# Kernel optimization log

Measured on AMD Instinct MI355X. Metric: run time of the kernel, lower is better.

## Reference

```python
import jax, jax.numpy as jnp
import numpy as np

B_SZ, NX, IN_DIM = 32, 16384, 3
DIM, J, MODE, RANK, FC_DIM, OUT_DIM, N_LAYERS = 64, 16, 128, 4, 128, 1, 3


def setup_inputs() -> dict:
    key = jax.random.key(0)
    ks = jax.random.split(key, 20)
    scale = 1.0 / (MODE * MODE)
    s_out = 1.0 / MODE
    x = jax.random.normal(ks[0], (B_SZ, NX, IN_DIM), jnp.float32)
    bases = jax.random.normal(ks[1], (NX, MODE), jnp.float32) / np.sqrt(NX)
    wbases = jax.random.normal(ks[2], (NX, MODE), jnp.float32) / np.sqrt(NX)
    product = bases.T @ wbases  # (MODE_out, MODE_in)
    D_out = np.sqrt(s_out) * jax.random.uniform(ks[3], (J, MODE), jnp.float32)
    D_in = np.sqrt(s_out) * jax.random.uniform(ks[4], (J, MODE), jnp.float32)
    A = s_out * jax.random.uniform(ks[5], (J, RANK, MODE), jnp.float32)
    Bm = s_out * jax.random.uniform(ks[6], (J, RANK, MODE), jnp.float32)
    W_sp = scale * jax.random.normal(ks[7], (N_LAYERS, DIM, DIM, J), jnp.float32)
    W_conv = jax.random.normal(ks[8], (N_LAYERS, DIM, DIM), jnp.float32) / np.sqrt(DIM)
    b_conv = jnp.zeros((N_LAYERS, DIM), jnp.float32)
    W0 = jax.random.normal(ks[9], (IN_DIM, DIM), jnp.float32) / np.sqrt(IN_DIM)
    b0 = jnp.zeros((DIM,), jnp.float32)
    W1 = jax.random.normal(ks[10], (DIM, FC_DIM), jnp.float32) / np.sqrt(DIM)
    b1 = jnp.zeros((FC_DIM,), jnp.float32)
    W2 = jax.random.normal(ks[11], (FC_DIM, OUT_DIM), jnp.float32) / np.sqrt(FC_DIM)
    b2 = jnp.zeros((OUT_DIM,), jnp.float32)
    return {"x": x, "bases": bases, "wbases": wbases, "product": product,
            "D_out": D_out, "D_in": D_in, "A": A, "Bm": Bm,
            "W_sp": W_sp, "W_conv": W_conv, "b_conv": b_conv,
            "W0": W0, "b0": b0, "W1": W1, "b1": b1, "W2": W2, "b2": b2}


def reference(x, bases, wbases, product, D_out, D_in, A, Bm, W_sp, W_conv, b_conv,
              W0, b0, W1, b1, W2, b2):
    # fc0: (b, nx, in_dim) -> (b, nx, dim), then channel-first (b, dim, nx)
    h = jnp.swapaxes(x @ W0 + b0, 1, 2)
    # H construction: diag outer-products + low-rank A^T B update (mask_mode=0 so full add)
    H = D_out[:, :, None] * D_in[:, None, :] * product[None] \
        + jnp.einsum('jrk,jrl->jkl', A, Bm)  # (J, MODE, MODE)
    for i in range(N_LAYERS):
        xh = jnp.einsum('bcx,xk->bck', h, wbases)          # spectral transform
        xh1 = jnp.einsum('jkl,bil->bijk', H, xh)           # H mixing
        y = jnp.einsum('ioj,bijk->bok', W_sp[i], xh1)      # channel/kernel contraction
        x1 = jnp.einsum('bck,xk->bcx', y, bases)           # inverse transform
        x2 = jnp.einsum('oc,bcx->box', W_conv[i], h) + b_conv[i][None, :, None]
        h = x1 + x2
        if i != N_LAYERS - 1:
            h = jax.nn.gelu(h, approximate=False)
    h = jnp.swapaxes(h, 1, 2)  # (b, nx, dim)
    h = jax.nn.gelu(h @ W1 + b1, approximate=False)
    return h @ W2 + b2
```

## Files before the change

kernel.cpp:

```cpp
#include <hip/hip_runtime.h>
#include <hip/hip_bf16.h>
#include <math.h>

#define B_SZ   32
#define NXX    16384
#define IN_DIM 3
#define DIM    64
#define JM     16
#define MODE   128
#define RANKK  4
#define FC_DIM 128
#define N_LAY  3

typedef __attribute__((ext_vector_type(8))) short bf16x8;
typedef __attribute__((ext_vector_type(4))) float f32x4;
typedef unsigned short u16;

__device__ __forceinline__ float gelu_fast(float v) {
    float p = v * (0.7978845608f + 0.0356774081f * v * v);
    float e = __expf(-2.f * p);
    return v * __builtin_amdgcn_rcpf(1.f + e);
}
__device__ __forceinline__ u16 to_bf16(float v) {
    __hip_bfloat16 b = __float2bfloat16(v);
    return *(u16*)&b;
}

__global__ __launch_bounds__(256) void k_zero(float* __restrict__ p, int n) {
    int i = blockIdx.x * 256 + threadIdx.x;
    if (i < n) p[i] = 0.f;
}

__global__ __launch_bounds__(256) void k_build_H(
        const float* __restrict__ Dout, const float* __restrict__ Din,
        const float* __restrict__ product, const float* __restrict__ A,
        const float* __restrict__ Bm, u16* __restrict__ Hbf) {
    int idx = blockIdx.x * 256 + threadIdx.x;
    int j = idx >> 14;
    int k = (idx >> 7) & 127;
    int l = idx & 127;
    float v = Dout[j * MODE + k] * Din[j * MODE + l] * product[k * MODE + l];
#pragma unroll
    for (int r = 0; r < RANKK; ++r)
        v += A[(j * RANKK + r) * MODE + k] * Bm[(j * RANKK + r) * MODE + l];
    Hbf[idx] = to_bf16(v);
}

__global__ __launch_bounds__(256) void k_setup_wst(
        const float* __restrict__ Wsp, u16* __restrict__ WsT) {
    int idx = blockIdx.x * 256 + threadIdx.x;
    int i = idx & 63, o = (idx >> 6) & 63, j = (idx >> 12) & 15, lay = idx >> 16;
    WsT[idx] = to_bf16(Wsp[(((size_t)lay * 64 + i) * 64 + o) * 16 + j]);
}

__global__ __launch_bounds__(256) void k_setup_bases(
        const float* __restrict__ bases, u16* __restrict__ bh) {
    int idx = blockIdx.x * 256 + threadIdx.x;
    int x = idx >> 7, k = idx & 127;
    size_t off = (size_t)(k >> 3) * 131072 + (size_t)x * 8 + (k & 7);
    bh[off] = to_bf16(bases[idx]);
}

__global__ __launch_bounds__(256) void k_setup_wbT(
        const float* __restrict__ wb, u16* __restrict__ Th) {
    __shared__ float tile[32][33];
    int bx = blockIdx.x, bl = blockIdx.y;
    int t = threadIdx.x;
    int i = t >> 5, jj = t & 31;
#pragma unroll
    for (int r = 0; r < 4; ++r)
        tile[i + r * 8][jj] = wb[(size_t)(bx * 32 + i + r * 8) * MODE + bl * 32 + jj];
    __syncthreads();
#pragma unroll
    for (int r = 0; r < 4; ++r) {
        int l = bl * 32 + i + r * 8;
        int x = bx * 32 + jj;
        Th[(size_t)l * NXX + x] = to_bf16(tile[jj][i + r * 8]);
    }
}

__global__ __launch_bounds__(256) void k_setup_w1t(
        const float* __restrict__ W1, u16* __restrict__ wh) {
    int i = blockIdx.x * 256 + threadIdx.x;
    int f = i >> 6, c = i & 63;
    wh[i] = to_bf16(W1[c * FC_DIM + f]);
}

__global__ __launch_bounds__(256) void k_fc0(
        const float* __restrict__ x, const float* __restrict__ W0,
        const float* __restrict__ b0, u16* __restrict__ hh) {
    __shared__ float w0s[IN_DIM * DIM + DIM];
    int t = threadIdx.x;
    if (t < IN_DIM * DIM) w0s[t] = W0[t];
    if (t < DIM) w0s[IN_DIM * DIM + t] = b0[t];
    __syncthreads();
    int b = blockIdx.y;
    int xi = blockIdx.x * 32 + (t >> 3);
    int c8 = (t & 7) * 8;
    const float* xp = x + ((size_t)b * NXX + xi) * IN_DIM;
    float x0 = xp[0], x1 = xp[1], x2 = xp[2];
    u16 rh[8];
#pragma unroll
    for (int i = 0; i < 8; ++i) {
        int c = c8 + i;
        float v = x0 * w0s[c] + x1 * w0s[DIM + c] + x2 * w0s[2 * DIM + c]
                + w0s[3 * DIM + c];
        rh[i] = to_bf16(v);
    }
    size_t o = ((size_t)(b << 14) + xi) * 64 + c8;
    *(ushort4*)(hh + o)     = make_ushort4(rh[0], rh[1], rh[2], rh[3]);
    *(ushort4*)(hh + o + 4) = make_ushort4(rh[4], rh[5], rh[6], rh[7]);
}

#define SPAD 72
__global__ __launch_bounds__(256) void k_spectral_mfma(
        const u16* __restrict__ Hh,
        const u16* __restrict__ Wh,
        float* __restrict__ xh) {
    __shared__ u16 Ash[64 * SPAD];
    int t = threadIdx.x;
    int wave = t >> 6, lane = t & 63, quad = lane >> 4, l16 = lane & 15;
    int b = blockIdx.x;
    int x0 = blockIdx.y * 512;
    int cq = (t & 15) * 4;
    int xq = (t >> 4) * 4;
    int colw = (xq + ((t & 7) << 3)) & 63;
    const u16* srch = Hh + ((size_t)(b << 14) + x0 + xq) * 64 + cq;
    int l0 = wave * 32;
    const u16* w0h = Wh + (size_t)(l0 + l16) * NXX + x0;
    const u16* w1h = Wh + (size_t)(l0 + 16 + l16) * NXX + x0;
    f32x4 acc[4][2] = {};
    for (int kt = 0; kt < 512; kt += 64) {
        __syncthreads();
        {
            const u16* s = srch + (size_t)kt * 64;
            ushort4 r0 = *(const ushort4*)(s);
            ushort4 r1 = *(const ushort4*)(s + 64);
            ushort4 r2 = *(const ushort4*)(s + 128);
            ushort4 r3 = *(const ushort4*)(s + 192);
            *(ushort4*)&Ash[(cq + 0) * SPAD + colw] = make_ushort4(r0.x, r1.x, r2.x, r3.x);
            *(ushort4*)&Ash[(cq + 1) * SPAD + colw] = make_ushort4(r0.y, r1.y, r2.y, r3.y);
            *(ushort4*)&Ash[(cq + 2) * SPAD + colw] = make_ushort4(r0.z, r1.z, r2.z, r3.z);
            *(ushort4*)&Ash[(cq + 3) * SPAD + colw] = make_ushort4(r0.w, r1.w, r2.w, r3.w);
        }
        __syncthreads();
#pragma unroll
        for (int k0 = 0; k0 < 64; k0 += 32) {
            bf16x8 afh[4];
#pragma unroll
            for (int ct = 0; ct < 4; ++ct) {
                int rr = ct * 16 + l16;
                int ro = rr * SPAD + (((k0 + quad * 8) + (((rr >> 2) & 7) << 3)) & 63);
                afh[ct] = *(const bf16x8*)&Ash[ro];
            }
            int go = kt + k0 + quad * 8;
            bf16x8 b0h = *(const bf16x8*)(w0h + go);
            bf16x8 b1h = *(const bf16x8*)(w1h + go);
#pragma unroll
            for (int ct = 0; ct < 4; ++ct) {
                acc[ct][0] = __builtin_amdgcn_mfma_f32_16x16x32_bf16(afh[ct], b0h, acc[ct][0], 0, 0, 0);
                acc[ct][1] = __builtin_amdgcn_mfma_f32_16x16x32_bf16(afh[ct], b1h, acc[ct][1], 0, 0, 0);
            }
        }
    }
    float* xb = xh + (size_t)(b << 6) * 128;
#pragma unroll
    for (int ct = 0; ct < 4; ++ct)
#pragma unroll
        for (int lt = 0; lt < 2; ++lt)
#pragma unroll
            for (int r = 0; r < 4; ++r)
                atomicAdd(xb + (size_t)(ct * 16 + quad * 4 + r) * 128 + l0 + lt * 16 + l16,
                          acc[ct][lt][r]);
}

#define XPAD 136
#define TPAD 72
__global__ __launch_bounds__(256) void k_hmix_mfma(
        const float* __restrict__ xh, const u16* __restrict__ Hbf,
        const u16* __restrict__ WsT, float* __restrict__ y, int lay) {
    __shared__ u16 xsb[64 * XPAD];
    __shared__ u16 Ts[128 * TPAD];
    int t = threadIdx.x;
    int wave = t >> 6, lane = t & 63, quad = lane >> 4, l16 = lane & 15;
    int b = blockIdx.x, j = blockIdx.y;
    const float* xb = xh + (size_t)b * DIM * MODE;
    for (int idx = t; idx < DIM * MODE; idx += 256)
        xsb[(idx >> 7) * XPAD + (idx & 127)] = to_bf16(xb[idx]);
    __syncthreads();
    int k_base = wave * 32;
    {
        f32x4 acc[2][4] = {};
        const u16* Hj = Hbf + (size_t)j * MODE * MODE;
#pragma unroll
        for (int l0 = 0; l0 < 128; l0 += 32) {
            bf16x8 af[2], bf[4];
#pragma unroll
            for (int mt = 0; mt < 2; ++mt)
                af[mt] = *(const bf16x8*)(Hj + (size_t)(k_base + mt * 16 + l16) * 128 + l0 + quad * 8);
#pragma unroll
            for (int nt = 0; nt < 4; ++nt)
                bf[nt] = *(const bf16x8*)&xsb[(nt * 16 + l16) * XPAD + l0 + quad * 8];
#pragma unroll
            for (int mt = 0; mt < 2; ++mt)
#pragma unroll
                for (int nt = 0; nt < 4; ++nt)
                    acc[mt][nt] = __builtin_amdgcn_mfma_f32_16x16x32_bf16(af[mt], bf[nt], acc[mt][nt], 0, 0, 0);
        }
#pragma unroll
        for (int mt = 0; mt < 2; ++mt)
#pragma unroll
            for (int nt = 0; nt < 4; ++nt)
#pragma unroll
                for (int r = 0; r < 4; ++r)
                    Ts[(k_base + mt * 16 + quad * 4 + r) * TPAD + nt * 16 + l16] =
                        to_bf16(acc[mt][nt][r]);
    }
    __syncthreads();
    {
        f32x4 acc[4][2] = {};
        const u16* Wj = WsT + ((size_t)lay * JM + j) * DIM * DIM;
#pragma unroll
        for (int i0 = 0; i0 < 64; i0 += 32) {
            bf16x8 af[4], bf[2];
#pragma unroll
            for (int mt = 0; mt < 4; ++mt)
                af[mt] = *(const bf16x8*)(Wj + (size_t)(mt * 16 + l16) * 64 + i0 + quad * 8);
#pragma unroll
            for (int nt = 0; nt < 2; ++nt)
                bf[nt] = *(const bf16x8*)&Ts[(k_base + nt * 16 + l16) * TPAD + i0 + quad * 8];
#pragma unroll
            for (int mt = 0; mt < 4; ++mt)
#pragma unroll
                for (int nt = 0; nt < 2; ++nt)
                    acc[mt][nt] = __builtin_amdgcn_mfma_f32_16x16x32_bf16(af[mt], bf[nt], acc[mt][nt], 0, 0, 0);
        }
        float* yb = y + (size_t)b * DIM * MODE;
#pragma unroll
        for (int mt = 0; mt < 4; ++mt)
#pragma unroll
            for (int nt = 0; nt < 2; ++nt)
#pragma unroll
                for (int r = 0; r < 4; ++r)
                    atomicAdd(yb + (size_t)(mt * 16 + quad * 4 + r) * 128 + k_base + nt * 16 + l16,
                              acc[mt][nt][r]);
    }
}

__global__ __launch_bounds__(256) void k_build_A(
        const float* __restrict__ y, const float* __restrict__ Wconv,
        u16* __restrict__ Ah, int lay) {
    int b = blockIdx.x;
    for (int idx = threadIdx.x; idx < 12288; idx += 256) {
        int i = idx & 7, l16 = (idx >> 3) & 15, quad = (idx >> 7) & 3,
            ot = (idx >> 9) & 3, ks = idx >> 11;
        int o = ot * 16 + l16;
        int k = ks * 32 + quad * 8 + i;
        float v = (k < 128) ? y[((size_t)b * DIM + o) * MODE + k]
                            : Wconv[(size_t)lay * DIM * DIM + o * DIM + (k - 128)];
        Ah[(size_t)b * 12288 + idx] = to_bf16(v);
    }
}

template <bool DO_MLP>
__global__ __launch_bounds__(256, 4) void k_inv_conv_mfma(
        const u16* __restrict__ Afh,
        const u16* __restrict__ Bfh,
        u16* __restrict__ Hh,
        const float* __restrict__ bconv, int lay,
        const u16* __restrict__ W1h,
        const float* __restrict__ b1, const float* __restrict__ W2,
        const float* __restrict__ b2, float* __restrict__ out) {
    __shared__ u16 Ash[12288];
    __shared__ u16 hsh[128 * 64];
    int t = threadIdx.x;
    int wave = t >> 6, lane = t & 63, quad = lane >> 4, l16 = lane & 15;
    int bid = blockIdx.x;
    int swz = (bid & 7) * 512 + (bid >> 3);
    int b = swz & 31;
    int x0 = (swz >> 5) * 128;

    const u16* afb = Afh + (size_t)b * 12288;
#pragma unroll
    for (int i = 0; i < 6; ++i) {
        int idx = i * 256 + t;
        *(bf16x8*)&Ash[idx * 8] = *(const bf16x8*)(afb + (size_t)idx * 8);
    }
#pragma unroll
    for (int it = 0; it < 4; ++it) {
        int idx = it * 256 + t;
        int row = idx >> 3, c8 = (idx & 7) * 8;
        size_t src = ((size_t)(b << 14) + x0 + row) * 64 + c8;
        *(bf16x8*)&hsh[row * 64 + (c8 ^ ((row & 7) << 3))] =
            *(const bf16x8*)(Hh + src);
    }
    __syncthreads();

    int xw = wave * 32;
    bf16x8 bglob[4][2];
#pragma unroll
    for (int ks = 0; ks < 4; ++ks)
#pragma unroll
        for (int x2 = 0; x2 < 2; ++x2) {
            int xl = xw + x2 * 16 + l16;
            size_t bo = (size_t)((ks * 4 + quad) * 16384 + x0 + xl) * 8;
            bglob[ks][x2] = *(const bf16x8*)(Bfh + bo);
        }

    f32x4 acc[4][2] = {};
#pragma unroll
    for (int ks = 0; ks < 6; ++ks) {
        bf16x8 afh[4], bfh[2];
#pragma unroll
        for (int x2 = 0; x2 < 2; ++x2) {
            if (ks < 4) {
                bfh[x2] = bglob[ks][x2];
            } else {
                int xl = xw + x2 * 16 + l16;
                int ko = (ks - 4) * 32 + quad * 8;
                bfh[x2] = *(const bf16x8*)&hsh[xl * 64 + (ko ^ ((xl & 7) << 3))];
            }
        }
#pragma unroll
        for (int ot = 0; ot < 4; ++ot)
            afh[ot] = *(const bf16x8*)&Ash[(((ks * 4 + ot) * 4 + quad) * 16 + l16) * 8];
#pragma unroll
        for (int ot = 0; ot < 4; ++ot)
#pragma unroll
            for (int x2 = 0; x2 < 2; ++x2)
                acc[ot][x2] = __builtin_amdgcn_mfma_f32_16x16x32_bf16(
                    afh[ot], bfh[x2], acc[ot][x2], 0, 0, 0);
    }

#pragma unroll
    for (int ot = 0; ot < 4; ++ot) {
        float4 bc = *(const float4*)(bconv + lay * DIM + ot * 16 + quad * 4);
#pragma unroll
        for (int x2 = 0; x2 < 2; ++x2) {
            int xl = xw + x2 * 16 + l16;
            float vr[4] = {acc[ot][x2][0] + bc.x, acc[ot][x2][1] + bc.y,
                           acc[ot][x2][2] + bc.z, acc[ot][x2][3] + bc.w};
            if (!DO_MLP) {
#pragma unroll
                for (int r = 0; r < 4; ++r) vr[r] = gelu_fast(vr[r]);
            }
            ushort4 uh;
            uh.x = to_bf16(vr[0]); uh.y = to_bf16(vr[1]);
            uh.z = to_bf16(vr[2]); uh.w = to_bf16(vr[3]);
            int col = ot * 16 + quad * 4;
            *(ushort4*)&hsh[xl * 64 + (col ^ ((xl & 7) << 3))] = uh;
        }
    }

    if (!DO_MLP) {
        __syncthreads();
#pragma unroll
        for (int it = 0; it < 4; ++it) {
            int idx = it * 256 + t;
            int row = idx >> 3, c8 = (idx & 7) * 8;
            size_t dst = ((size_t)(b << 14) + x0 + row) * 64 + c8;
            *(bf16x8*)(Hh + dst) =
                *(const bf16x8*)&hsh[row * 64 + (c8 ^ ((row & 7) << 3))];
        }
        return;
    }

#pragma unroll
    for (int x2 = 0; x2 < 2; ++x2) {
        int xl = xw + x2 * 16 + l16;
        bf16x8 ah[2];
#pragma unroll
        for (int ks = 0; ks < 2; ++ks) {
            int ko = ks * 32 + quad * 8;
            ah[ks] = *(const bf16x8*)&hsh[xl * 64 + (ko ^ ((xl & 7) << 3))];
        }
        float vo[4] = {0.f, 0.f, 0.f, 0.f};
#pragma unroll
        for (int ft = 0; ft < 8; ++ft) {
            f32x4 a2 = {};
#pragma unroll
            for (int ks = 0; ks < 2; ++ks) {
                size_t o = (size_t)(ft * 16 + l16) * 64 + ks * 32 + quad * 8;
                bf16x8 bh = *(const bf16x8*)(W1h + o);
                a2 = __builtin_amdgcn_mfma_f32_16x16x32_bf16(ah[ks], bh, a2, 0, 0, 0);
            }
            float bb = b1[ft * 16 + l16];
            float w2 = W2[ft * 16 + l16];
#pragma unroll
            for (int r = 0; r < 4; ++r)
                vo[r] += gelu_fast(a2[r] + bb) * w2;
        }
#pragma unroll
        for (int r = 0; r < 4; ++r) {
            float v = vo[r];
            v += __shfl_xor(v, 1);
            v += __shfl_xor(v, 2);
            v += __shfl_xor(v, 4);
            v += __shfl_xor(v, 8);
            vo[r] = v;
        }
        if (l16 == 0) {
            float bb2 = b2[0];
            float4 o4 = make_float4(vo[0] + bb2, vo[1] + bb2,
                                    vo[2] + bb2, vo[3] + bb2);
            *(float4*)(out + (size_t)b * NXX + x0 + xw + x2 * 16 + quad * 4) = o4;
        }
    }
}

extern "C" void kernel_launch(void* const* d_in, const int* in_sizes, int n_in,
                              void* d_out, int out_size, void* d_ws, size_t ws_size,
                              hipStream_t stream) {
    const float* x      = (const float*)d_in[0];
    const float* bases  = (const float*)d_in[1];
    const float* wbases = (const float*)d_in[2];
    const float* product= (const float*)d_in[3];
    const float* Dout   = (const float*)d_in[4];
    const float* Din    = (const float*)d_in[5];
    const float* A      = (const float*)d_in[6];
    const float* Bm     = (const float*)d_in[7];
    const float* Wsp    = (const float*)d_in[8];
    const float* Wconv  = (const float*)d_in[9];
    const float* bconv  = (const float*)d_in[10];
    const float* W0     = (const float*)d_in[11];
    const float* b0     = (const float*)d_in[12];
    const float* W1     = (const float*)d_in[13];
    const float* b1     = (const float*)d_in[14];
    const float* W2     = (const float*)d_in[15];
    const float* b2     = (const float*)d_in[16];
    float* out = (float*)d_out;

    const size_t need = 79314944;
    if (ws_size < need) {
        k_zero<<<dim3((out_size + 255) / 256), dim3(256), 0, stream>>>(out, out_size);
        return;
    }

    char* W = (char*)d_ws;
    size_t off = 0;
    auto alloc = [&](size_t bytes) { void* p = W + off; off += bytes; return p; };
    u16*   Hbf      = (u16*)alloc(524288);
    u16*   WsT      = (u16*)alloc(393216);
    u16*   bases_hi = (u16*)alloc(4194304);
    u16*   wbT_hi   = (u16*)alloc(4194304);
    u16*   Abuf_hi  = (u16*)alloc(786432);
    float* ybuf     = (float*)alloc(1048576);
    float* xh       = (float*)alloc(1048576);
    u16*   h_hi     = (u16*)alloc(67108864);
    u16*   w1t_hi   = (u16*)alloc(16384);

    k_build_H<<<dim3(1024), dim3(256), 0, stream>>>(Dout, Din, product, A, Bm, Hbf);
    k_setup_wst<<<dim3(768), dim3(256), 0, stream>>>(Wsp, WsT);
    k_setup_bases<<<dim3(8192), dim3(256), 0, stream>>>(bases, bases_hi);
    k_setup_wbT<<<dim3(512, 4), dim3(256), 0, stream>>>(wbases, wbT_hi);
    k_setup_w1t<<<dim3(32), dim3(256), 0, stream>>>(W1, w1t_hi);
    k_fc0<<<dim3(512, B_SZ), dim3(256), 0, stream>>>(x, W0, b0, h_hi);

    for (int lay = 0; lay < N_LAY; ++lay) {
        int last = (lay == N_LAY - 1);
        k_zero<<<dim3(2048), dim3(256), 0, stream>>>(ybuf, 524288);
        k_spectral_mfma<<<dim3(B_SZ, 32), dim3(256), 0, stream>>>(
            h_hi, wbT_hi, xh);
        k_hmix_mfma<<<dim3(B_SZ, JM), dim3(256), 0, stream>>>(
            xh, Hbf, WsT, ybuf, lay);
        k_build_A<<<dim3(B_SZ), dim3(256), 0, stream>>>(ybuf, Wconv, Abuf_hi, lay);
        dim3 g(4096), blk(256);
        if (last)
            k_inv_conv_mfma<true><<<g, blk, 0, stream>>>(
                Abuf_hi, bases_hi, h_hi, bconv, lay,
                w1t_hi, b1, W2, b2, out);
        else
            k_inv_conv_mfma<false><<<g, blk, 0, stream>>>(
                Abuf_hi, bases_hi, h_hi, bconv, lay,
                w1t_hi, b1, W2, b2, out);
    }
}
```

Measured before the change: 473.9 us.

## Fuse H-mixing with A-buffer build and double-tile the inverse conv kernel

The H-mixing kernel now loops over all 16 kernel indices inside one block per batch. It accumulates y in registers and writes the bf16 A-operand layout directly, which removes the y atomics, the y zeroing kernel and the separate k_build_A launch. The inverse-transform/conv kernel now handles two 128-column tiles per block. It loads the h operand straight from global memory into registers and prefetches the second tile while the first tile's epilogue runs. The trade-off is that H-mixing drops to only 32 blocks running a serial j loop, which may leave most compute units idle, and xh is now zeroed explicitly before the spectral step.

```diff
diff --git a/kernel.cpp b/kernel.cpp
--- a/kernel.cpp
+++ b/kernel.cpp
@@ -176,90 +176,86 @@
 
 #define XPAD 136
 #define TPAD 72
-__global__ __launch_bounds__(256) void k_hmix_mfma(
+__global__ __launch_bounds__(256) void k_hmix2(
         const float* __restrict__ xh, const u16* __restrict__ Hbf,
-        const u16* __restrict__ WsT, float* __restrict__ y, int lay) {
+        const u16* __restrict__ WsT, const float* __restrict__ Wconv,
+        u16* __restrict__ Ah, int lay) {
     __shared__ u16 xsb[64 * XPAD];
     __shared__ u16 Ts[128 * TPAD];
     int t = threadIdx.x;
     int wave = t >> 6, lane = t & 63, quad = lane >> 4, l16 = lane & 15;
-    int b = blockIdx.x, j = blockIdx.y;
+    int b = blockIdx.x;
     const float* xb = xh + (size_t)b * DIM * MODE;
     for (int idx = t; idx < DIM * MODE; idx += 256)
         xsb[(idx >> 7) * XPAD + (idx & 127)] = to_bf16(xb[idx]);
+    for (int idx = 8192 + t; idx < 12288; idx += 256) {
+        int i = idx & 7, ll = (idx >> 3) & 15, qq = (idx >> 7) & 3,
+            ot = (idx >> 9) & 3, ks = idx >> 11;
+        int o = ot * 16 + ll;
+        int k = ks * 32 + qq * 8 + i;
+        Ah[(size_t)b * 12288 + idx] =
+            to_bf16(Wconv[(size_t)lay * DIM * DIM + o * DIM + (k - 128)]);
+    }
     __syncthreads();
     int k_base = wave * 32;
-    {
-        f32x4 acc[2][4] = {};
-        const u16* Hj = Hbf + (size_t)j * MODE * MODE;
-#pragma unroll
-        for (int l0 = 0; l0 < 128; l0 += 32) {
-            bf16x8 af[2], bf[4];
+    f32x4 accy[4][2] = {};
+    for (int j = 0; j < JM; ++j) {
+        {
+            f32x4 acc[2][4] = {};
+            const u16* Hj = Hbf + (size_t)j * MODE * MODE;
+#pragma unroll
+            for (int l0 = 0; l0 < 128; l0 += 32) {
+                bf16x8 af[2], bf[4];
+#pragma unroll
+                for (int mt = 0; mt < 2; ++mt)
+                    af[mt] = *(const bf16x8*)(Hj + (size_t)(k_base + mt * 16 + l16) * 128 + l0 + quad * 8);
+#pragma unroll
+                for (int nt = 0; nt < 4; ++nt)
+                    bf[nt] = *(const bf16x8*)&xsb[(nt * 16 + l16) * XPAD + l0 + quad * 8];
+#pragma unroll
+                for (int mt = 0; mt < 2; ++mt)
+#pragma unroll
+                    for (int nt = 0; nt < 4; ++nt)
+                        acc[mt][nt] = __builtin_amdgcn_mfma_f32_16x16x32_bf16(af[mt], bf[nt], acc[mt][nt], 0, 0, 0);
+            }
 #pragma unroll
             for (int mt = 0; mt < 2; ++mt)
-                af[mt] = *(const bf16x8*)(Hj + (size_t)(k_base + mt * 16 + l16) * 128 + l0 + quad * 8);
-#pragma unroll
-            for (int nt = 0; nt < 4; ++nt)
-                bf[nt] = *(const bf16x8*)&xsb[(nt * 16 + l16) * XPAD + l0 + quad * 8];
-#pragma unroll
-            for (int mt = 0; mt < 2; ++mt)
 #pragma unroll
                 for (int nt = 0; nt < 4; ++nt)
-                    acc[mt][nt] = __builtin_amdgcn_mfma_f32_16x16x32_bf16(af[mt], bf[nt], acc[mt][nt], 0, 0, 0);
-        }
-#pragma unroll
-        for (int mt = 0; mt < 2; ++mt)
-#pragma unroll
-            for (int nt = 0; nt < 4; ++nt)
-#pragma unroll
-                for (int r = 0; r < 4; ++r)
-                    Ts[(k_base + mt * 16 + quad * 4 + r) * TPAD + nt * 16 + l16] =
-                        to_bf16(acc[mt][nt][r]);
-    }
-    __syncthreads();
-    {
-        f32x4 acc[4][2] = {};
-        const u16* Wj = WsT + ((size_t)lay * JM + j) * DIM * DIM;
-#pragma unroll
-        for (int i0 = 0; i0 < 64; i0 += 32) {
-            bf16x8 af[4], bf[2];
-#pragma unroll
-            for (int mt = 0; mt < 4; ++mt)
-                af[mt] = *(const bf16x8*)(Wj + (size_t)(mt * 16 + l16) * 64 + i0 + quad * 8);
-#pragma unroll
-            for (int nt = 0; nt < 2; ++nt)
-                bf[nt] = *(const bf16x8*)&Ts[(k_base + nt * 16 + l16) * TPAD + i0 + quad * 8];
-#pragma unroll
-            for (int mt = 0; mt < 4; ++mt)
+#pragma unroll
+                    for (int r = 0; r < 4; ++r)
+                        Ts[(k_base + mt * 16 + quad * 4 + r) * TPAD + nt * 16 + l16] =
+                            to_bf16(acc[mt][nt][r]);
+        }
+        {
+            const u16* Wj = WsT + ((size_t)lay * JM + j) * DIM * DIM;
+#pragma unroll
+            for (int i0 = 0; i0 < 64; i0 += 32) {
+                bf16x8 af[4], bf[2];
+#pragma unroll
+                for (int mt = 0; mt < 4; ++mt)
+                    af[mt] = *(const bf16x8*)(Wj + (size_t)(mt * 16 + l16) * 64 + i0 + quad * 8);
 #pragma unroll
                 for (int nt = 0; nt < 2; ++nt)
-                    acc[mt][nt] = __builtin_amdgcn_mfma_f32_16x16x32_bf16(af[mt], bf[nt], acc[mt][nt], 0, 0, 0);
-        }
-        float* yb = y + (size_t)b * DIM * MODE;
-#pragma unroll
-        for (int mt = 0; mt < 4; ++mt)
-#pragma unroll
-            for (int nt = 0; nt < 2; ++nt)
-#pragma unroll
-                for (int r = 0; r < 4; ++r)
-                    atomicAdd(yb + (size_t)(mt * 16 + quad * 4 + r) * 128 + k_base + nt * 16 + l16,
-                              acc[mt][nt][r]);
-    }
-}
-
-__global__ __launch_bounds__(256) void k_build_A(
-        const float* __restrict__ y, const float* __restrict__ Wconv,
-        u16* __restrict__ Ah, int lay) {
-    int b = blockIdx.x;
-    for (int idx = threadIdx.x; idx < 12288; idx += 256) {
-        int i = idx & 7, l16 = (idx >> 3) & 15, quad = (idx >> 7) & 3,
-            ot = (idx >> 9) & 3, ks = idx >> 11;
-        int o = ot * 16 + l16;
-        int k = ks * 32 + quad * 8 + i;
-        float v = (k < 128) ? y[((size_t)b * DIM + o) * MODE + k]
-                            : Wconv[(size_t)lay * DIM * DIM + o * DIM + (k - 128)];
-        Ah[(size_t)b * 12288 + idx] = to_bf16(v);
-    }
+                    bf[nt] = *(const bf16x8*)&Ts[(k_base + nt * 16 + l16) * TPAD + i0 + quad * 8];
+#pragma unroll
+                for (int mt = 0; mt < 4; ++mt)
+#pragma unroll
+                    for (int nt = 0; nt < 2; ++nt)
+                        accy[mt][nt] = __builtin_amdgcn_mfma_f32_16x16x32_bf16(af[mt], bf[nt], accy[mt][nt], 0, 0, 0);
+            }
+        }
+    }
+#pragma unroll
+    for (int mt = 0; mt < 4; ++mt)
+#pragma unroll
+        for (int nt = 0; nt < 2; ++nt)
+#pragma unroll
+            for (int r = 0; r < 4; ++r) {
+                int idx = (((wave * 4 + mt) * 4 + nt * 2 + (l16 >> 3)) * 16
+                           + quad * 4 + r) * 8 + (l16 & 7);
+                Ah[(size_t)b * 12288 + idx] = to_bf16(accy[mt][nt][r]);
+            }
 }
 
 template <bool DO_MLP>
@@ -272,13 +268,14 @@
         const float* __restrict__ b1, const float* __restrict__ W2,
         const float* __restrict__ b2, float* __restrict__ out) {
     __shared__ u16 Ash[12288];
-    __shared__ u16 hsh[128 * 64];
+    __shared__ u16 osh[128 * 64];
     int t = threadIdx.x;
     int wave = t >> 6, lane = t & 63, quad = lane >> 4, l16 = lane & 15;
     int bid = blockIdx.x;
-    int swz = (bid & 7) * 512 + (bid >> 3);
+    int swz = (bid & 7) * 256 + (bid >> 3);
     int b = swz & 31;
-    int x0 = (swz >> 5) * 128;
+    int x0 = (swz >> 5) * 256;
+    int xw = wave * 32;
 
     const u16* afb = Afh + (size_t)b * 12288;
 #pragma unroll
@@ -286,126 +283,143 @@
         int idx = i * 256 + t;
         *(bf16x8*)&Ash[idx * 8] = *(const bf16x8*)(afb + (size_t)idx * 8);
     }
-#pragma unroll
-    for (int it = 0; it < 4; ++it) {
-        int idx = it * 256 + t;
-        int row = idx >> 3, c8 = (idx & 7) * 8;
-        size_t src = ((size_t)(b << 14) + x0 + row) * 64 + c8;
-        *(bf16x8*)&hsh[row * 64 + (c8 ^ ((row & 7) << 3))] =
-            *(const bf16x8*)(Hh + src);
-    }
-    __syncthreads();
-
-    int xw = wave * 32;
-    bf16x8 bglob[4][2];
-#pragma unroll
-    for (int ks = 0; ks < 4; ++ks)
-#pragma unroll
-        for (int x2 = 0; x2 < 2; ++x2) {
-            int xl = xw + x2 * 16 + l16;
-            size_t bo = (size_t)((ks * 4 + quad) * 16384 + x0 + xl) * 8;
-            bglob[ks][x2] = *(const bf16x8*)(Bfh + bo);
-        }
-
-    f32x4 acc[4][2] = {};
-#pragma unroll
-    for (int ks = 0; ks < 6; ++ks) {
-        bf16x8 afh[4], bfh[2];
-#pragma unroll
-        for (int x2 = 0; x2 < 2; ++x2) {
-            if (ks < 4) {
-                bfh[x2] = bglob[ks][x2];
-            } else {
+
+    auto loadB = [&](int x0t, bf16x8 (&bg)[4][2], bf16x8 (&hf)[2][2]) {
+#pragma unroll
+        for (int ks = 0; ks < 4; ++ks)
+#pragma unroll
+            for (int x2 = 0; x2 < 2; ++x2) {
                 int xl = xw + x2 * 16 + l16;
-                int ko = (ks - 4) * 32 + quad * 8;
-                bfh[x2] = *(const bf16x8*)&hsh[xl * 64 + (ko ^ ((xl & 7) << 3))];
-            }
-        }
-#pragma unroll
-        for (int ot = 0; ot < 4; ++ot)
-            afh[ot] = *(const bf16x8*)&Ash[(((ks * 4 + ot) * 4 + quad) * 16 + l16) * 8];
-#pragma unroll
-        for (int ot = 0; ot < 4; ++ot)
-#pragma unroll
-            for (int x2 = 0; x2 < 2; ++x2)
-                acc[ot][x2] = __builtin_amdgcn_mfma_f32_16x16x32_bf16(
-                    afh[ot], bfh[x2], acc[ot][x2], 0, 0, 0);
-    }
-
-#pragma unroll
-    for (int ot = 0; ot < 4; ++ot) {
-        float4 bc = *(const float4*)(bconv + lay * DIM + ot * 16 + quad * 4);
-#pragma unroll
-        for (int x2 = 0; x2 < 2; ++x2) {
-            int xl = xw + x2 * 16 + l16;
-            float vr[4] = {acc[ot][x2][0] + bc.x, acc[ot][x2][1] + bc.y,
-                           acc[ot][x2][2] + bc.z, acc[ot][x2][3] + bc.w};
-            if (!DO_MLP) {
-#pragma unroll
-                for (int r = 0; r < 4; ++r) vr[r] = gelu_fast(vr[r]);
-            }
-            ushort4 uh;
-            uh.x = to_bf16(vr[0]); uh.y = to_bf16(vr[1]);
-            uh.z = to_bf16(vr[2]); uh.w = to_bf16(vr[3]);
-            int col = ot * 16 + quad * 4;
-            *(ushort4*)&hsh[xl * 64 + (col ^ ((xl & 7) << 3))] = uh;
-        }
-    }
-
-    if (!DO_MLP) {
+                bg[ks][x2] = *(const bf16x8*)(Bfh + (size_t)((ks * 4 + quad) * 16384 + x0t + xl) * 8);
+            }
+#pragma unroll
+        for (int ks = 0; ks < 2; ++ks)
+#pragma unroll
+            for (int x2 = 0; x2 < 2; ++x2) {
+                int xl = xw + x2 * 16 + l16;
+                hf[ks][x2] = *(const bf16x8*)(Hh + ((size_t)(b << 14) + x0t + xl) * 64
+                                              + ks * 32 + quad * 8);
+            }
+    };
+
+    auto ksloop = [&](const bf16x8 (&bg)[4][2], const bf16x8 (&hf)[2][2],
+                      f32x4 (&acc)[4][2]) {
+#pragma unroll
+        for (int ks = 0; ks < 6; ++ks) {
+            bf16x8 afh[4];
+#pragma unroll
+            for (int ot = 0; ot < 4; ++ot)
+                afh[ot] = *(const bf16x8*)&Ash[(((ks * 4 + ot) * 4 + quad) * 16 + l16) * 8];
+#pragma unroll
+            for (int ot = 0; ot < 4; ++ot)
+#pragma unroll
+                for (int x2 = 0; x2 < 2; ++x2)
+                    acc[ot][x2] = __builtin_amdgcn_mfma_f32_16x16x32_bf16(
+                        afh[ot], ks < 4 ? bg[ks][x2] : hf[ks - 4][x2],
+                        acc[ot][x2], 0, 0, 0);
+        }
+    };
+
+    auto epi_store = [&](int x0t, f32x4 (&acc)[4][2], bool lastTile) {
+#pragma unroll
+        for (int ot = 0; ot < 4; ++ot) {
+            float4 bc = *(const float4*)(bconv + lay * DIM + ot * 16 + quad * 4);
+#pragma unroll
+            for (int x2 = 0; x2 < 2; ++x2) {
+                int xl = xw + x2 * 16 + l16;
+                ushort4 uh;
+                uh.x = to_bf16(gelu_fast(acc[ot][x2][0] + bc.x));
+                uh.y = to_bf16(gelu_fast(acc[ot][x2][1] + bc.y));
+                uh.z = to_bf16(gelu_fast(acc[ot][x2][2] + bc.z));
+                uh.w = to_bf16(gelu_fast(acc[ot][x2][3] + bc.w));
+                int col = ot * 16 + quad * 4;
+                *(ushort4*)&osh[xl * 64 + (col ^ ((xl & 7) << 3))] = uh;
+            }
+        }
         __syncthreads();
 #pragma unroll
         for (int it = 0; it < 4; ++it) {
             int idx = it * 256 + t;
             int row = idx >> 3, c8 = (idx & 7) * 8;
-            size_t dst = ((size_t)(b << 14) + x0 + row) * 64 + c8;
+            size_t dst = ((size_t)(b << 14) + x0t + row) * 64 + c8;
             *(bf16x8*)(Hh + dst) =
-                *(const bf16x8*)&hsh[row * 64 + (c8 ^ ((row & 7) << 3))];
-        }
-        return;
-    }
-
-#pragma unroll
-    for (int x2 = 0; x2 < 2; ++x2) {
-        int xl = xw + x2 * 16 + l16;
-        bf16x8 ah[2];
-#pragma unroll
-        for (int ks = 0; ks < 2; ++ks) {
-            int ko = ks * 32 + quad * 8;
-            ah[ks] = *(const bf16x8*)&hsh[xl * 64 + (ko ^ ((xl & 7) << 3))];
-        }
-        float vo[4] = {0.f, 0.f, 0.f, 0.f};
-#pragma unroll
-        for (int ft = 0; ft < 8; ++ft) {
-            f32x4 a2 = {};
+                *(const bf16x8*)&osh[row * 64 + (c8 ^ ((row & 7) << 3))];
+        }
+        if (!lastTile) __syncthreads();
+    };
+
+    auto epi_mlp = [&](int x0t, f32x4 (&acc)[4][2]) {
+#pragma unroll
+        for (int ot = 0; ot < 4; ++ot) {
+            float4 bc = *(const float4*)(bconv + lay * DIM + ot * 16 + quad * 4);
+#pragma unroll
+            for (int x2 = 0; x2 < 2; ++x2) {
+                int xl = xw + x2 * 16 + l16;
+                ushort4 uh;
+                uh.x = to_bf16(acc[ot][x2][0] + bc.x);
+                uh.y = to_bf16(acc[ot][x2][1] + bc.y);
+                uh.z = to_bf16(acc[ot][x2][2] + bc.z);
+                uh.w = to_bf16(acc[ot][x2][3] + bc.w);
+                int col = ot * 16 + quad * 4;
+                *(ushort4*)&osh[xl * 64 + (col ^ ((xl & 7) << 3))] = uh;
+            }
+        }
+#pragma unroll
+        for (int x2 = 0; x2 < 2; ++x2) {
+            int xl = xw + x2 * 16 + l16;
+            bf16x8 ah[2];
 #pragma unroll
             for (int ks = 0; ks < 2; ++ks) {
-                size_t o = (size_t)(ft * 16 + l16) * 64 + ks * 32 + quad * 8;
-                bf16x8 bh = *(const bf16x8*)(W1h + o);
-                a2 = __builtin_amdgcn_mfma_f32_16x16x32_bf16(ah[ks], bh, a2, 0, 0, 0);
-            }
-            float bb = b1[ft * 16 + l16];
-            float w2 = W2[ft * 16 + l16];
-#pragma unroll
-            for (int r = 0; r < 4; ++r)
-                vo[r] += gelu_fast(a2[r] + bb) * w2;
-        }
-#pragma unroll
-        for (int r = 0; r < 4; ++r) {
-            float v = vo[r];
-            v += __shfl_xor(v, 1);
-            v += __shfl_xor(v, 2);
-            v += __shfl_xor(v, 4);
-            v += __shfl_xor(v, 8);
-            vo[r] = v;
-        }
-        if (l16 == 0) {
-            float bb2 = b2[0];
-            float4 o4 = make_float4(vo[0] + bb2, vo[1] + bb2,
-                                    vo[2] + bb2, vo[3] + bb2);
-            *(float4*)(out + (size_t)b * NXX + x0 + xw + x2 * 16 + quad * 4) = o4;
-        }
-    }
+                int ko = ks * 32 + quad * 8;
+                ah[ks] = *(const bf16x8*)&osh[xl * 64 + (ko ^ ((xl & 7) << 3))];
+            }
+            float vo[4] = {0.f, 0.f, 0.f, 0.f};
+#pragma unroll
+            for (int ft = 0; ft < 8; ++ft) {
+                f32x4 a2 = {};
+#pragma unroll
+                for (int ks = 0; ks < 2; ++ks) {
+                    size_t o = (size_t)(ft * 16 + l16) * 64 + ks * 32 + quad * 8;
+                    bf16x8 bh = *(const bf16x8*)(W1h + o);
+                    a2 = __builtin_amdgcn_mfma_f32_16x16x32_bf16(ah[ks], bh, a2, 0, 0, 0);
+                }
+                float bb = b1[ft * 16 + l16];
+                float w2 = W2[ft * 16 + l16];
+#pragma unroll
+                for (int r = 0; r < 4; ++r)
+                    vo[r] += gelu_fast(a2[r] + bb) * w2;
+            }
+#pragma unroll
+            for (int r = 0; r < 4; ++r) {
+                float v = vo[r];
+                v += __shfl_xor(v, 1);
+                v += __shfl_xor(v, 2);
+                v += __shfl_xor(v, 4);
+                v += __shfl_xor(v, 8);
+                vo[r] = v;
+            }
+            if (l16 == 0) {
+                float bb2 = b2[0];
+                float4 o4 = make_float4(vo[0] + bb2, vo[1] + bb2,
+                                        vo[2] + bb2, vo[3] + bb2);
+                *(float4*)(out + (size_t)b * NXX + x0t + xw + x2 * 16 + quad * 4) = o4;
+            }
+        }
+    };
+
+    bf16x8 bgA[4][2], hfA[2][2];
+    loadB(x0, bgA, hfA);
+    __syncthreads();
+    f32x4 acc[4][2] = {};
+    ksloop(bgA, hfA, acc);
+    bf16x8 bgB[4][2], hfB[2][2];
+    loadB(x0 + 128, bgB, hfB);
+    if (!DO_MLP) epi_store(x0, acc, false);
+    else         epi_mlp(x0, acc);
+    f32x4 acc2[4][2] = {};
+    ksloop(bgB, hfB, acc2);
+    if (!DO_MLP) epi_store(x0 + 128, acc2, true);
+    else         epi_mlp(x0 + 128, acc2);
 }
 
 extern "C" void kernel_launch(void* const* d_in, const int* in_sizes, int n_in,
@@ -448,6 +462,7 @@
     float* xh       = (float*)alloc(1048576);
     u16*   h_hi     = (u16*)alloc(67108864);
     u16*   w1t_hi   = (u16*)alloc(16384);
+    (void)ybuf;
 
     k_build_H<<<dim3(1024), dim3(256), 0, stream>>>(Dout, Din, product, A, Bm, Hbf);
     k_setup_wst<<<dim3(768), dim3(256), 0, stream>>>(Wsp, WsT);
@@ -458,13 +473,12 @@
 
     for (int lay = 0; lay < N_LAY; ++lay) {
         int last = (lay == N_LAY - 1);
-        k_zero<<<dim3(2048), dim3(256), 0, stream>>>(ybuf, 524288);
+        k_zero<<<dim3(1024), dim3(256), 0, stream>>>(xh, 262144);
         k_spectral_mfma<<<dim3(B_SZ, 32), dim3(256), 0, stream>>>(
             h_hi, wbT_hi, xh);
-        k_hmix_mfma<<<dim3(B_SZ, JM), dim3(256), 0, stream>>>(
-            xh, Hbf, WsT, ybuf, lay);
-        k_build_A<<<dim3(B_SZ), dim3(256), 0, stream>>>(ybuf, Wconv, Abuf_hi, lay);
-        dim3 g(4096), blk(256);
+        k_hmix2<<<dim3(B_SZ), dim3(256), 0, stream>>>(
+            xh, Hbf, WsT, Wconv, Abuf_hi, lay);
+        dim3 g(2048), blk(256);
         if (last)
             k_inv_conv_mfma<true><<<g, blk, 0, stream>>>(
                 Abuf_hi, bases_hi, h_hi, bconv, lay,
```

Result: slower. 507.4 us (+7.1%).
